# Kernel tuning notes

Hardware: AMD Instinct MI355X
Metric: run time of the kernel (lower is better)

Reference implementation:

```python
import jax, jax.numpy as jnp
import numpy as np

N, FIN, H, M = 20000, 64, 128, 16
EIA, EIR, EIT = 256000, 256000, 100000
EIN = 2 * H + 1          # EGNN edge-mlp input: feats_i | feats_j | rel_dist
EHID = 2 * EIN
NIN = H + M
NHID = 2 * H


def _gat(x_src, x_dst, ei, w_src, w_dst, a_s, a_d, b):
    # PyG GATConv, heads=1: alpha_ij = softmax_i(leaky_relu(a_s.Wx_j + a_d.Wx_i))
    n_dst = x_dst.shape[0]
    h_s = x_src @ w_src                      # [Ns, H]
    h_d = x_dst @ w_dst                      # [Nd, H]
    es = h_s @ a_s                           # [Ns]
    ed = h_d @ a_d                           # [Nd]
    j, i = ei[0], ei[1]                      # src, dst
    e = jax.nn.leaky_relu(es[j] + ed[i], 0.2)
    mx = jax.ops.segment_max(e, i, num_segments=n_dst)
    mx = jnp.where(jnp.isfinite(mx), mx, 0.0)  # guard empty segments
    ex = jnp.exp(e - mx[i])
    den = jax.ops.segment_sum(ex, i, num_segments=n_dst)
    alpha = ex / (den[i] + 1e-16)
    return jax.ops.segment_sum(alpha[:, None] * h_s[j], i, num_segments=n_dst) + b


def _egnn(x, ei, p):
    # EGNN_Sparse: x = [coors(3) | feats], 'add' aggregation, residual feat update
    ew1, eb1, ew2, eb2, cw1, cb1, cw2, cb2, nw1, nb1, nw2, nb2 = p
    coors, feats = x[:, :3], x[:, 3:]
    n = x.shape[0]
    j, i = ei[0], ei[1]
    rel = coors[j] - coors[i]                          # [E, 3] (src - dst)
    rd = jnp.sum(rel * rel, axis=-1, keepdims=True)    # [E, 1]
    m_in = jnp.concatenate([feats[i], feats[j], rd], axis=-1)
    m = jax.nn.silu(jax.nn.silu(m_in @ ew1 + eb1) @ ew2 + eb2)   # [E, M]
    cw = jax.nn.silu(m @ cw1 + cb1) @ cw2 + cb2                  # [E, 1]
    coors_out = coors + jax.ops.segment_sum(cw * rel, i, num_segments=n)
    m_i = jax.ops.segment_sum(m, i, num_segments=n)
    feats_out = feats + jax.nn.silu(jnp.concatenate([feats, m_i], axis=-1) @ nw1 + nb1) @ nw2 + nb2
    return jnp.concatenate([coors_out, feats_out], axis=-1)


def setup_inputs():
    ks = iter(jax.random.split(jax.random.key(0), 48))

    def nrm(shape, s=0.1):
        return jax.random.normal(next(ks), shape, dtype=jnp.float32) * s

    def ridx(shape):
        return jax.random.randint(next(ks), shape, 0, N, dtype=jnp.int32)

    return {
        "x1": nrm((N, FIN), 1.0), "x2": nrm((N, FIN), 1.0),
        "pos1": nrm((N, 3), 1.0), "pos2": nrm((N, 3), 1.0),
        "ei_intra1": ridx((2, EIA)), "ei_intra2": ridx((2, EIA)),
        "ei_12": ridx((2, EIR)), "ei_21": ridx((2, EIR)),
        "ei_int": ridx((2, EIT)),
        "g0_w": nrm((2, FIN, H)), "g0_as": nrm((2, H)), "g0_ad": nrm((2, H)), "g0_b": nrm((2, H)),
        "g1_w": nrm((2, H, H)), "g1_as": nrm((2, H)), "g1_ad": nrm((2, H)), "g1_b": nrm((2, H)),
        "it_ws": nrm((2, 2, H, H)), "it_wd": nrm((2, 2, H, H)),
        "it_as": nrm((2, 2, H)), "it_ad": nrm((2, 2, H)), "it_b": nrm((2, 2, H)),
        "eg_e_w1": nrm((2, 2, EIN, EHID)), "eg_e_b1": nrm((2, 2, EHID)),
        "eg_e_w2": nrm((2, 2, EHID, M)), "eg_e_b2": nrm((2, 2, M)),
        "eg_c_w1": nrm((2, 2, M, 4 * M)), "eg_c_b1": nrm((2, 2, 4 * M)),
        "eg_c_w2": nrm((2, 2, 4 * M, 1)), "eg_c_b2": nrm((2, 2, 1)),
        "eg_n_w1": nrm((2, 2, NIN, NHID)), "eg_n_b1": nrm((2, 2, NHID)),
        "eg_n_w2": nrm((2, 2, NHID, H)), "eg_n_b2": nrm((2, 2, H)),
        "lin_w": nrm((H, 1)), "lin_b": nrm((1,)),
        "aux_w1": nrm((2 * H, H)), "aux_b1": nrm((H,)),
        "aux_w2": nrm((H, 1)), "aux_b2": nrm((1,)),
    }


def reference(x1, x2, pos1, pos2,
              g0_w, g0_as, g0_ad, g0_b, g1_w, g1_as, g1_ad, g1_b,
              it_ws, it_wd, it_as, it_ad, it_b,
              eg_e_w1, eg_e_b1, eg_e_w2, eg_e_b2, eg_c_w1, eg_c_b1, eg_c_w2, eg_c_b2,
              eg_n_w1, eg_n_b1, eg_n_w2, eg_n_b2,
              lin_w, lin_b, aux_w1, aux_b1, aux_w2, aux_b2,
              ei_intra1, ei_intra2, ei_12, ei_21, ei_int):
    n1, n2 = x1.shape[0], x2.shape[0]
    sl1 = jnp.tile(jnp.arange(n1, dtype=ei_intra1.dtype)[None, :], (2, 1))
    sl2 = jnp.tile(jnp.arange(n2, dtype=ei_intra2.dtype)[None, :], (2, 1))
    ei1 = jnp.concatenate([ei_intra1, sl1], axis=1)  # GATConv add_self_loops=True
    ei2 = jnp.concatenate([ei_intra2, sl2], axis=1)
    # intra GAT layers (shared lin for src/dst)
    x1 = jax.nn.relu(_gat(x1, x1, ei1, g0_w[0], g0_w[0], g0_as[0], g0_ad[0], g0_b[0]))
    x2 = jax.nn.relu(_gat(x2, x2, ei2, g0_w[1], g0_w[1], g0_as[1], g0_ad[1], g0_b[1]))
    x1 = jax.nn.relu(_gat(x1, x1, ei1, g1_w[0], g1_w[0], g1_as[0], g1_ad[0], g1_b[0]))
    x2 = jax.nn.relu(_gat(x2, x2, ei2, g1_w[1], g1_w[1], g1_as[1], g1_ad[1], g1_b[1]))
    # inter GAT layers (bipartite, add_self_loops=False)
    for l in range(2):
        nx2 = jax.nn.relu(_gat(x1, x2, ei_12, it_ws[l, 0], it_wd[l, 0], it_as[l, 0], it_ad[l, 0], it_b[l, 0]))
        nx1 = jax.nn.relu(_gat(x2, x1, ei_21, it_ws[l, 1], it_wd[l, 1], it_as[l, 1], it_ad[l, 1], it_b[l, 1]))
        x1, x2 = nx1, nx2
    # EGNN layers (HeteroEGNN hstacks pos only when feat dim == node_dim, i.e. layer 0)
    egp = (eg_e_w1, eg_e_b1, eg_e_w2, eg_e_b2, eg_c_w1, eg_c_b1, eg_c_w2, eg_c_b2,
           eg_n_w1, eg_n_b1, eg_n_w2, eg_n_b2)
    h1 = jnp.concatenate([pos1, x1], axis=-1)
    h2 = jnp.concatenate([pos2, x2], axis=-1)
    for l in range(2):
        h1 = _egnn(h1, ei_intra1, tuple(p[l, 0] for p in egp))
        h2 = _egnn(h2, ei_intra2, tuple(p[l, 1] for p in egp))
    x1, x2 = h1[:, 3:], h2[:, 3:]
    # auxiliary distance head on interacting pairs
    xi = jnp.concatenate([x1[ei_int[0]], x2[ei_int[1]]], axis=-1)
    dist = jax.nn.relu(jax.nn.relu(xi @ aux_w1 + aux_b1) @ aux_w2 + aux_b2)
    return (x1 @ lin_w + lin_b, x2 @ lin_w + lin_b, dist)
```

## Files before the change

kernel.cpp:

```cpp
#include <hip/hip_runtime.h>
#include <hip/hip_bf16.h>
#include <cstdint>
#include <cstddef>

#define NN     20000
#define FIN_D  64
#define H_D    128
#define M_D    16
#define EIA_D  256000
#define EIR_D  256000
#define EIT_D  100000
#define EIN_D  257
#define EHID_D 514
#define NIN_D  144
#define NHID_D 256
#define APAD   544
#define BUPAD  272

typedef short bfrag __attribute__((ext_vector_type(8)));
typedef float ffrag __attribute__((ext_vector_type(4)));

__device__ __forceinline__ float siluf(float x) {
    return x * __builtin_amdgcn_rcpf(1.f + __expf(-x));
}
// ... 86 lines not shown
        lo[idx] = f2bf(v - bf2f(h));
    }
}

struct MMJob {
    const float* A; const float* A2;
    const int* gi0; const int* gi1;
    const unsigned short* Wh; const unsigned short* Wl;
    const float* bias; const float* res;
    float* C; unsigned short* C2;
    const float* da; const float* db;
    float* dota; float* dotb;
};
struct MMJobs { MMJob j[4]; };

template<int ACT, bool RES, bool OBF, bool GATHER, bool DUAL, int AMODE, int DOT, bool NOC>
__global__ __launch_bounds__(256) void k_mm(MMJobs js, int M, int Nc, int K, int Kpad, int ldc, int s2) {
    __shared__ __align__(16) unsigned short sAh[128 * 32];
    __shared__ __align__(16) unsigned short sAl[AMODE == 2 ? 128 * 32 : 16];
    const MMJob jb = js.j[blockIdx.z];
    const int tid = threadIdx.x;
    const int bm = blockIdx.x * 128, bn = blockIdx.y * 64;
    const int wv = tid >> 6, lane = tid & 63;
    ffrag acc[2][4];
#pragma unroll
    for (int mt = 0; mt < 2; ++mt)
#pragma unroll
        for (int nt = 0; nt < 4; ++nt)
#pragma unroll
            for (int r = 0; r < 4; ++r) acc[mt][nt][r] = 0.f;
    const int sr = tid >> 1;
    const int sks = (tid & 1) * 16;
    const int gm_s = bm + sr;
    const int sgmt = sr >> 4, smm = sr & 15, qb = (tid & 1) * 2;
// ... 13 lines not shown
#pragma unroll
            for (int i = 0; i < 4; ++i) {
                float4 t4 = ((const float4*)src)[i];
                v[4 * i] = t4.x; v[4 * i + 1] = t4.y; v[4 * i + 2] = t4.z; v[4 * i + 3] = t4.w;
            }
        } else {
#pragma unroll
            for (int i = 0; i < 16; ++i) v[i] = 0.f;
        }
#pragma unroll
        for (int o = 0; o < 2; ++o) {
            unsigned hw[4], lw[4];
#pragma unroll
            for (int p = 0; p < 4; ++p) {
                float f0 = v[o * 8 + 2 * p], f1 = v[o * 8 + 2 * p + 1];
                if (AMODE == 2) {
                    unsigned short h0 = f2bf(f0), h1 = f2bf(f1);
                    unsigned short l0 = f2bf(f0 - bf2f(h0)), l1 = f2bf(f1 - bf2f(h1));
                    hw[p] = (unsigned)h0 | ((unsigned)h1 << 16);
                    lw[p] = (unsigned)l0 | ((unsigned)l1 << 16);
                } else {
                    hw[p] = pkbf(f0, f1);
                }
            }
            int off16 = (sgmt * 4 + qb + o) * 16 + smm;
            ((uint4*)sAh)[off16] = make_uint4(hw[0], hw[1], hw[2], hw[3]);
            if (AMODE == 2) ((uint4*)sAl)[off16] = make_uint4(lw[0], lw[1], lw[2], lw[3]);
        }
        __syncthreads();
        bfrag bh[4], bl[4];
#pragma unroll
        for (int nt = 0; nt < 4; ++nt) {
            size_t woff = (size_t)(bn + nt * 16 + mm) * Kpad + k0 + q * 8;
            bh[nt] = *(const bfrag*)(jb.Wh + woff);
            bl[nt] = *(const bfrag*)(jb.Wl + woff);
        }
#pragma unroll
        for (int mt = 0; mt < 2; ++mt) {
            int off16 = ((wv * 2 + mt) * 4 + q) * 16 + mm;
            bfrag ah = ((const bfrag*)sAh)[off16];
#pragma unroll
            for (int nt = 0; nt < 4; ++nt) {
                acc[mt][nt] = __builtin_amdgcn_mfma_f32_16x16x32_bf16(ah, bh[nt], acc[mt][nt], 0, 0, 0);
                acc[mt][nt] = __builtin_amdgcn_mfma_f32_16x16x32_bf16(ah, bl[nt], acc[mt][nt], 0, 0, 0);
            }
            if (AMODE == 2) {
                bfrag al = ((const bfrag*)sAl)[off16];
#pragma unroll
                for (int nt = 0; nt < 4; ++nt)
                    acc[mt][nt] = __builtin_amdgcn_mfma_f32_16x16x32_bf16(al, bh[nt], acc[mt][nt], 0, 0, 0);
            }
        }
        __syncthreads();
    }
    if (DOT >= 1) {
        float dav[4], dbv[4];
#pragma unroll
        for (int nt = 0; nt < 4; ++nt) {
            int gn = bn + nt * 16 + mm;
            dav[nt] = (gn < Nc) ? jb.da[gn] : 0.f;
            if (DOT == 2) dbv[nt] = (gn < Nc) ? jb.db[gn] : 0.f;
        }
#pragma unroll
        for (int mt = 0; mt < 2; ++mt)
#pragma unroll
            for (int r = 0; r < 4; ++r) {
                int gm = bm + wv * 32 + mt * 16 + q * 4 + r;
                float sa = 0.f, sb = 0.f;
#pragma unroll
                for (int nt = 0; nt < 4; ++nt) {
                    sa += acc[mt][nt][r] * dav[nt];
                    if (DOT == 2) sb += acc[mt][nt][r] * dbv[nt];
                }
                sa += __shfl_xor(sa, 1); sa += __shfl_xor(sa, 2);
                sa += __shfl_xor(sa, 4); sa += __shfl_xor(sa, 8);
                if (DOT == 2) {
                    sb += __shfl_xor(sb, 1); sb += __shfl_xor(sb, 2);
                    sb += __shfl_xor(sb, 4); sb += __shfl_xor(sb, 8);
                }
                if (mm == 0 && gm < M) {
                    atomicAdd(jb.dota + gm, sa);
                    if (DOT == 2) atomicAdd(jb.dotb + gm, sb);
                }
            }
    }
    if (!NOC || DUAL) {
#pragma unroll
        for (int mt = 0; mt < 2; ++mt) {
#pragma unroll
            for (int nt = 0; nt < 4; ++nt) {
                int gn = bn + nt * 16 + mm;
                bool inb = gn < Nc;
                bool padz = OBF && !NOC && !inb && gn < ldc;
                if (!inb && !padz) continue;
#pragma unroll
                for (int r = 0; r < 4; ++r) {
                    int gm = bm + wv * 32 + mt * 16 + q * 4 + r;
                    if (gm >= M) continue;
                    if (padz) {
                        ((unsigned short*)jb.C)[(size_t)gm * ldc + gn] = 0;
                        continue;
                    }
                    float vv = acc[mt][nt][r];
                    if (jb.bias) vv += jb.bias[gn];
                    if (ACT == 1) vv = reluf(vv);
                    if (ACT == 2) vv = siluf(vv);
                    if (RES) vv += jb.res[(size_t)gm * Nc + gn];
                    if (!NOC) {
                        if (OBF) ((unsigned short*)jb.C)[(size_t)gm * ldc + gn] = f2bf(vv);
                        else jb.C[(size_t)gm * ldc + gn] = vv;
                    }
                    if (DUAL) jb.C2[(size_t)gm * ldc + gn] = f2bf(vv);
                }
            }
        }
    }
}

__global__ void k_nodescore(const float* __restrict__ x, const float* __restrict__ wv,
                            const float* __restrict__ b, float* __restrict__ o, int n) {
    int w = blockIdx.x * 4 + (threadIdx.x >> 6);
    int lane = threadIdx.x & 63;
    if (w >= n) return;
    const float* r = x + (size_t)w * H_D;
    float s = r[lane] * wv[lane] + r[lane + 64] * wv[lane + 64];
#pragma unroll
    for (int off = 32; off; off >>= 1) s += __shfl_xor(s, off);
    if (lane == 0) o[w] = s + b[0];
}

__global__ __launch_bounds__(256) void k_gat_fused(
        const int* __restrict__ rp, const int* __restrict__ cj, int hasSelf,
        const float* __restrict__ es, const float* __restrict__ ed,
        const unsigned* __restrict__ h16, const float* __restrict__ bias,
        float* __restrict__ out, int N) {
    int node = blockIdx.x * 4 + (threadIdx.x >> 6);
    int lane = threadIdx.x & 63;
    if (node >= N) return;
    int start = rp[node], end = rp[node + 1];
    float edi = ed[node];
    float den = 0.f, a0 = 0.f, a1 = 0.f;
    int p = start;
    for (; p + 2 <= end; p += 2) {
        int j0 = cj[p], j1 = cj[p + 1];
        float e0 = es[j0], e1 = es[j1];
        unsigned u0 = h16[(size_t)j0 * 64 + lane];
        unsigned u1 = h16[(size_t)j1 * 64 + lane];
        float v0 = e0 + edi; v0 = v0 < 0.f ? 0.2f * v0 : v0;
        float v1 = e1 + edi; v1 = v1 < 0.f ? 0.2f * v1 : v1;
        float x0 = __expf(v0), x1 = __expf(v1);
        den += x0 + x1;
        a0 += x0 * bf_lo(u0) + x1 * bf_lo(u1);
        a1 += x0 * bf_hi(u0) + x1 * bf_hi(u1);
    }
    if (p < end) {
        int j = cj[p];
        float v = es[j] + edi;
        v = v < 0.f ? 0.2f * v : v;
        float ex = __expf(v);
        den += ex;
        unsigned u = h16[(size_t)j * 64 + lane];
        a0 += ex * bf_lo(u);
        a1 += ex * bf_hi(u);
    }
    if (hasSelf) {
        float v = es[node] + edi;
        v = v < 0.f ? 0.2f * v : v;
        float ex = __expf(v);
        den += ex;
        unsigned u = h16[(size_t)node * 64 + lane];
        a0 += ex * bf_lo(u);
        a1 += ex * bf_hi(u);
    }
    float inv = 1.f / (den + 1e-16f);
    float2 o;
    o.x = reluf(a0 * inv + bias[2 * lane]);
    o.y = reluf(a1 * inv + bias[2 * lane + 1]);
    ((float2*)(out + (size_t)node * H_D))[lane] = o;
}

__global__ __launch_bounds__(256) void k_edge_mfma(
        const int* __restrict__ dsti, const int* __restrict__ cj, int nE,
        const unsigned* __restrict__ A16, const unsigned* __restrict__ Bp,
        const float* __restrict__ coors,
        const float* __restrict__ w_rd,
        const unsigned short* __restrict__ Wfh, const unsigned short* __restrict__ Wfl,
        const float* __restrict__ eb2,
        const float* __restrict__ cw1, const float* __restrict__ cb1,
        const float* __restrict__ cw2, const float* __restrict__ cb2,
        unsigned short* __restrict__ me16, float* __restrict__ cvec) {
    __shared__ __align__(16) float s_w[APAD];
    __shared__ float s_cw1[1024];
    __shared__ float s_cb1[64], s_cw2[64], s_eb2[16];
    __shared__ float sM[4][16][17];
    for (int i = threadIdx.x; i < APAD; i += 256)
        s_w[i] = (i < EHID_D) ? w_rd[i] : 0.f;
    for (int i = threadIdx.x; i < 1024; i += 256) s_cw1[i] = cw1[i];
    if (threadIdx.x < 64) { s_cb1[threadIdx.x] = cb1[threadIdx.x]; s_cw2[threadIdx.x] = cw2[threadIdx.x]; }
    if (threadIdx.x < 16) s_eb2[threadIdx.x] = eb2[threadIdx.x];
    __syncthreads();
    const float cb2v = cb2[0];
    const int wv = threadIdx.x >> 6, lane = threadIdx.x & 63;
    const int q = lane >> 4, mm = lane & 15;
    const int ebase = blockIdx.x * 64 + wv * 16;
    const int e = ebase + mm;
    const bool ev = e < nE;
    int ii = ev ? dsti[e] : 0;
    int jj = ev ? cj[e] : 0;
    float dx = coors[(size_t)jj * 3]     - coors[(size_t)ii * 3];
    float dy = coors[(size_t)jj * 3 + 1] - coors[(size_t)ii * 3 + 1];
    float dz = coors[(size_t)jj * 3 + 2] - coors[(size_t)ii * 3 + 2];
    float rd = dx * dx + dy * dy + dz * dz;
    const unsigned* Ar = A16 + (size_t)ii * BUPAD;
    const unsigned* Br = Bp + (size_t)jj * BUPAD;
    ffrag acc = {0.f, 0.f, 0.f, 0.f};
#pragma unroll 4
    for (int t = 0; t < 17; ++t) {
        int ks = t * 32 + q * 8;
        int ku = ks >> 1;
        uint4 au = *(const uint4*)(Ar + ku);
        uint4 bu = *(const uint4*)(Br + ku);
        float4 w0 = *(const float4*)(s_w + ks);
        float4 w1 = *(const float4*)(s_w + ks + 4);
        float g[8];
        g[0] = siluf(bf_lo(au.x) + bf_lo(bu.x) + rd * w0.x);
        g[1] = siluf(bf_hi(au.x) + bf_hi(bu.x) + rd * w0.y);
        g[2] = siluf(bf_lo(au.y) + bf_lo(bu.y) + rd * w0.z);
        g[3] = siluf(bf_hi(au.y) + bf_hi(bu.y) + rd * w0.w);
        g[4] = siluf(bf_lo(au.z) + bf_lo(bu.z) + rd * w1.x);
        g[5] = siluf(bf_hi(au.z) + bf_hi(bu.z) + rd * w1.y);
        g[6] = siluf(bf_lo(au.w) + bf_lo(bu.w) + rd * w1.z);
        g[7] = siluf(bf_hi(au.w) + bf_hi(bu.w) + rd * w1.w);
        bfrag ah;
        unsigned* ahp = (unsigned*)&ah;
        ahp[0] = pkbf(g[0], g[1]);
        ahp[1] = pkbf(g[2], g[3]);
        ahp[2] = pkbf(g[4], g[5]);
        ahp[3] = pkbf(g[6], g[7]);
        bfrag bh = *(const bfrag*)(Wfh + (size_t)(t * 64 + lane) * 8);
        bfrag bl = *(const bfrag*)(Wfl + (size_t)(t * 64 + lane) * 8);
        acc = __builtin_amdgcn_mfma_f32_16x16x32_bf16(ah, bh, acc, 0, 0, 0);
        acc = __builtin_amdgcn_mfma_f32_16x16x32_bf16(ah, bl, acc, 0, 0, 0);
    }
#pragma unroll
    for (int r = 0; r < 4; ++r) {
        int erow = q * 4 + r;
        float me = siluf(acc[r] + s_eb2[mm]);
        sM[wv][erow][mm] = me;
        int e2 = ebase + erow;
        if (e2 < nE) me16[(size_t)e2 * 16 + mm] = f2bf(me);
    }
    for (int el = 0; el < 16; ++el) {
        int e3 = ebase + el;
        if (e3 >= nE) break;
        float a = s_cb1[lane];
#pragma unroll
        for (int c = 0; c < 16; ++c) a += sM[wv][el][c] * s_cw1[c * 64 + lane];
        float p = siluf(a) * s_cw2[lane];
#pragma unroll
        for (int off = 32; off; off >>= 1) p += __shfl_xor(p, off);
        float cwv = p + cb2v;
        if (lane == el) {
            cvec[(size_t)e3 * 3]     = cwv * dx;
            cvec[(size_t)e3 * 3 + 1] = cwv * dy;
            cvec[(size_t)e3 * 3 + 2] = cwv * dz;
        }
    }
}

__global__ __launch_bounds__(256) void k_egnn_seg(
        const int* __restrict__ rp,
        const unsigned short* __restrict__ me16, const float* __restrict__ cvec,
        const float* __restrict__ coors,
        float* __restrict__ coorsOut, float* __restrict__ macc, int N) {
    int node = blockIdx.x * 4 + (threadIdx.x >> 6);
    int lane = threadIdx.x & 63;
    if (node >= N) return;
    int s = rp[node], en = rp[node + 1];
    int x = lane >> 4, c = lane & 15;
    float msum = 0.f, csum = 0.f;
    for (int p = s + x; p < en; p += 4) {
        msum += bf2f(me16[(size_t)p * 16 + c]);
        if (c < 3) csum += cvec[(size_t)p * 3 + c];
    }
    msum += __shfl_xor(msum, 16); msum += __shfl_xor(msum, 32);
    csum += __shfl_xor(csum, 16); csum += __shfl_xor(csum, 32);
    if (lane < 16) macc[(size_t)node * M_D + lane] = msum;
    if (lane < 3) coorsOut[(size_t)node * 3 + lane] = coors[(size_t)node * 3 + lane] + csum;
}

__global__ void k_dist(const float* __restrict__ Hb, const float* __restrict__ w2,
                       const float* __restrict__ b2, float* __restrict__ dist, int nE) {
    int e = blockIdx.x * 4 + (threadIdx.x >> 6);
    int lane = threadIdx.x & 63;
    if (e >= nE) return;
    const float* r = Hb + (size_t)e * H_D;
    float s = r[lane] * w2[lane] + r[lane + 64] * w2[lane + 64];
#pragma unroll
    for (int off = 32; off; off >>= 1) s += __shfl_xor(s, off);
    if (lane == 0) dist[e] = reluf(s + b2[0]);
}

extern "C" void kernel_launch(void* const* d_in, const int* in_sizes, int n_in,
// ... 124 lines not shown
    k_hist<<<gEA, 256, 0, stream>>>(ei_21 + EIR_D, EIR_D, cnt4 + 3 * N);
    k_scan4<<<4, 256, 0, stream>>>(cnt4, N, rp4);
    k_filli<<<(4 * N + 255) / 256, 256, 0, stream>>>(cnt4, 0, 4 * N);
    const int* rpI1 = rp4;
    const int* rpI2 = rp4 + (N + 1);
    const int* rp12 = rp4 + 2 * (N + 1);
    const int* rp21 = rp4 + 3 * (N + 1);
    k_scatter<<<gEA, 256, 0, stream>>>(ei_intra1, ei_intra1 + EIA_D, EIA_D, rpI1, cnt4, cjI1, dstI1);
    k_scatter<<<gEA, 256, 0, stream>>>(ei_intra2, ei_intra2 + EIA_D, EIA_D, rpI2, cnt4 + N, cjI2, dstI2);
    k_scatter<<<gEA, 256, 0, stream>>>(ei_12, ei_12 + EIR_D, EIR_D, rp12, cnt4 + 2 * N, cj12, nullptr);
    k_scatter<<<gEA, 256, 0, stream>>>(ei_21, ei_21 + EIR_D, EIR_D, rp21, cnt4 + 3 * N, cj21, nullptr);

    const int MB = (N + 127) / 128;
    MMJobs js{};

    auto intra = [&](const float* xa, const float* xb, int wa, int wb,
                     const float* as_a, const float* ad_a, const float* as_b, const float* ad_b,
                     const float* b_a, const float* b_b, int K, float* oa, float* ob) {
        int Kpad = (K + 31) & ~31;
        k_filli<<<(4 * N + 255) / 256, 256, 0, stream>>>((int*)esed, 0, 4 * N);
        js.j[0] = {xa, nullptr, nullptr, nullptr, WH(wa), WL(wa), nullptr, nullptr,
                   nullptr, (unsigned short*)h16a, as_a, ad_a, es1, ed1};
        js.j[1] = {xb, nullptr, nullptr, nullptr, WH(wb), WL(wb), nullptr, nullptr,
                   nullptr, (unsigned short*)h16b, as_b, ad_b, es2, ed2};
        k_mm<0, false, false, false, true, 1, 2, true><<<dim3(MB, 2, 2), 256, 0, stream>>>(
            js, N, H, K, Kpad, H, 0);
        k_gat_fused<<<gNW, 256, 0, stream>>>(rpI1, cjI1, 1, es1, ed1, h16a, b_a, oa, N);
        k_gat_fused<<<gNW, 256, 0, stream>>>(rpI2, cjI2, 1, es2, ed2, h16b, b_b, ob, N);
    };

    intra(x1_in, x2_in, 0, 1, g0_as, g0_ad, g0_as + H, g0_ad + H, g0_b, g0_b + H, FIN_D, x1a, x2a);
    const float* cx1 = x1a;
    const float* cx2 = x2a;
    intra(cx1, cx2, 2, 3, g1_as, g1_ad, g1_as + H, g1_ad + H, g1_b, g1_b + H, H, x1b, x2b);
    cx1 = x1b; cx2 = x2b;

    {
        float* outs1[2] = {x1a, x1b};
        float* outs2[2] = {x2a, x2b};
        for (int l = 0; l < 2; ++l) {
            int p0 = l * 2 + 0, p1 = l * 2 + 1;
            float* o2 = outs2[l];
            float* o1 = outs1[l];
            k_filli<<<(4 * N + 255) / 256, 256, 0, stream>>>((int*)esed, 0, 4 * N);
            js.j[0] = {cx1, nullptr, nullptr, nullptr, WH(4 + p0), WL(4 + p0), nullptr, nullptr,
                       nullptr, (unsigned short*)h16a, it_as + p0 * H, nullptr, es1, nullptr};
            js.j[1] = {cx2, nullptr, nullptr, nullptr, WH(4 + p1), WL(4 + p1), nullptr, nullptr,
                       nullptr, (unsigned short*)h16b, it_as + p1 * H, nullptr, es2, nullptr};
            k_mm<0, false, false, false, true, 1, 1, true><<<dim3(MB, 2, 2), 256, 0, stream>>>(
                js, N, H, H, H, H, 0);
            js.j[0] = {cx2, nullptr, nullptr, nullptr, WH(8 + p0), WL(8 + p0), nullptr, nullptr,
                       nullptr, nullptr, it_ad + p0 * H, nullptr, ed1, nullptr};
            js.j[1] = {cx1, nullptr, nullptr, nullptr, WH(8 + p1), WL(8 + p1), nullptr, nullptr,
                       nullptr, nullptr, it_ad + p1 * H, nullptr, ed2, nullptr};
            k_mm<0, false, false, false, false, 1, 1, true><<<dim3(MB, 2, 2), 256, 0, stream>>>(
                js, N, H, H, H, H, 0);
            k_gat_fused<<<gNW, 256, 0, stream>>>(rp12, cj12, 0, es1, ed1, h16a, it_b + p0 * H, o2, N);
            k_gat_fused<<<gNW, 256, 0, stream>>>(rp21, cj21, 0, es2, ed2, h16b, it_b + p1 * H, o1, N);
            cx1 = o1; cx2 = o2;
        }
    }

    auto egnn_pair = [&](const float* f1, const float* f2, const float* c1, const float* c2,
                         int l, float* fo1, float* fo2, float* co1, float* co2) {
        int p0 = 2 * l, p1 = 2 * l + 1;
        js.j[0] = {f1, nullptr, nullptr, nullptr, WH(12 + 2 * p0), WL(12 + 2 * p0),
                   eg_e_b1 + p0 * EHID_D, nullptr, (float*)A16a, nullptr, nullptr, nullptr, nullptr, nullptr};
        js.j[1] = {f1, nullptr, nullptr, nullptr, WH(13 + 2 * p0), WL(13 + 2 * p0),
                   nullptr, nullptr, (float*)B16a, nullptr, nullptr, nullptr, nullptr, nullptr};
        js.j[2] = {f2, nullptr, nullptr, nullptr, WH(12 + 2 * p1), WL(12 + 2 * p1),
                   eg_e_b1 + p1 * EHID_D, nullptr, (float*)A16b, nullptr, nullptr, nullptr, nullptr, nullptr};
        js.j[3] = {f2, nullptr, nullptr, nullptr, WH(13 + 2 * p1), WL(13 + 2 * p1),
                   nullptr, nullptr, (float*)B16b, nullptr, nullptr, nullptr, nullptr, nullptr};
        k_mm<0, false, true, false, false, 1, 0, false><<<dim3(MB, 9, 4), 256, 0, stream>>>(
            js, N, EHID_D, H, H, APAD, 0);
        const float* ew1a = eg_e_w1 + (size_t)p0 * EIN_D * EHID_D;
        const float* ew1b = eg_e_w1 + (size_t)p1 * EIN_D * EHID_D;
        k_edge_mfma<<<(EIA_D + 63) / 64, 256, 0, stream>>>(
            dstI1, cjI1, EIA_D, A16a, B16a, c1, ew1a + (size_t)256 * EHID_D,
            Wf + (size_t)p0 * 8704, Wf + 4 * 8704 + (size_t)p0 * 8704,
            eg_e_b2 + p0 * M_D, eg_c_w1 + p0 * M_D * 64, eg_c_b1 + p0 * 64,
            eg_c_w2 + p0 * 64, eg_c_b2 + p0, me16a, cveca);
        k_edge_mfma<<<(EIA_D + 63) / 64, 256, 0, stream>>>(
            dstI2, cjI2, EIA_D, A16b, B16b, c2, ew1b + (size_t)256 * EHID_D,
            Wf + (size_t)p1 * 8704, Wf + 4 * 8704 + (size_t)p1 * 8704,
            eg_e_b2 + p1 * M_D, eg_c_w1 + p1 * M_D * 64, eg_c_b1 + p1 * 64,
            eg_c_w2 + p1 * 64, eg_c_b2 + p1, me16b, cvecb);
        k_egnn_seg<<<gNW, 256, 0, stream>>>(rpI1, me16a, cveca, c1, co1, macc1, N);
        k_egnn_seg<<<gNW, 256, 0, stream>>>(rpI2, me16b, cvecb, c2, co2, macc2, N);
        js.j[0] = {f1, macc1, iota, iota, WH(20 + p0), WL(20 + p0),
                   eg_n_b1 + p0 * NHID_D, nullptr, nh1, nullptr, nullptr, nullptr, nullptr, nullptr};
        js.j[1] = {f2, macc2, iota, iota, WH(20 + p1), WL(20 + p1),
                   eg_n_b1 + p1 * NHID_D, nullptr, nh2, nullptr, nullptr, nullptr, nullptr, nullptr};
        k_mm<2, false, false, true, false, 2, 0, false><<<dim3(MB, 4, 2), 256, 0, stream>>>(
            js, N, NHID_D, NIN_D, 160, NHID_D, M_D);
        js.j[0] = {nh1, nullptr, nullptr, nullptr, WH(24 + p0), WL(24 + p0),
                   eg_n_b2 + p0 * H, f1, fo1, nullptr, nullptr, nullptr, nullptr, nullptr};
        js.j[1] = {nh2, nullptr, nullptr, nullptr, WH(24 + p1), WL(24 + p1),
                   eg_n_b2 + p1 * H, f2, fo2, nullptr, nullptr, nullptr, nullptr, nullptr};
        k_mm<0, true, false, false, false, 2, 0, false><<<dim3(MB, 2, 2), 256, 0, stream>>>(
            js, N, H, NHID_D, NHID_D, H, 0);
    };
    egnn_pair(cx1, cx2, pos1, pos2, 0, x1a, x2a, co1a, co2a);
    cx1 = x1a; cx2 = x2a;
    egnn_pair(cx1, cx2, co1a, co2a, 1, x1b, x2b, co1b, co2b);
    cx1 = x1b; cx2 = x2b;

    k_nodescore<<<gNW, 256, 0, stream>>>(cx1, lin_w, lin_b, dout, N);
    k_nodescore<<<gNW, 256, 0, stream>>>(cx2, lin_w, lin_b, dout + N, N);
    js.j[0] = {cx1, cx2, ei_int, ei_int + EIT_D, WH(28), WL(28),
               aux_b1, nullptr, Hb, nullptr, nullptr, nullptr, nullptr, nullptr};
    k_mm<1, false, false, true, false, 2, 0, false><<<dim3((EIT_D + 127) / 128, 2, 1), 256, 0, stream>>>(
        js, EIT_D, H, 2 * H, 2 * H, H, H_D);
    k_dist<<<(EIT_D + 3) / 4, 256, 0, stream>>>(Hb, aux_w2, aux_b2, dout + 2 * N, EIT_D);
}
```

Before: 1.601 ms.

## Add full-K resident GEMM kernel and batch paired GAT/edge/segment launches

Adds k_mmf, which stages the whole 128-row A tile in shared memory once and loops over all N-column blocks inside one workgroup. This lets the attention dot products be written directly, removing the zero-fill kernels and atomics. The paired GAT, EGNN edge and segment kernels now launch once each, with a 2-wide grid dimension selecting the job, which cuts launch count. The GAT aggregation loop is unrolled by 4 to put more gathers in flight. The trade-off is fewer workgroups per GEMM (grid y becomes 1), so each block does more serial work and parallelism drops.

```diff
diff --git a/kernel.cpp b/kernel.cpp
--- a/kernel.cpp
+++ b/kernel.cpp
@@ -124,10 +124,151 @@
 };
 struct MMJobs { MMJob j[4]; };
 
-template<int ACT, bool RES, bool OBF, bool GATHER, bool DUAL, int AMODE, int DOT, bool NOC>
+template<int ACT, bool OBF, int DOT, bool NOC, int KT>
+__global__ __launch_bounds__(256) void k_mmf(MMJobs js, int M, int Nc, int ldc, int nbn) {
+    constexpr int K = KT * 32;
+    __shared__ __align__(16) unsigned short sAh[128 * K];
+    const MMJob jb = js.j[blockIdx.z];
+    const int tid = threadIdx.x;
+    const int bm = blockIdx.x * 128;
+    const int wv = tid >> 6, lane = tid & 63;
+    const int q = lane >> 4, mm = lane & 15;
+    const int sr = tid >> 1;
+    const int sks = (tid & 1) * 16;
+    const int gm_s = bm + sr;
+    const int sgmt = sr >> 4, smm = sr & 15, qb = (tid & 1) * 2;
+#pragma unroll
+    for (int t = 0; t < KT; ++t) {
+        float v[16];
+        if (gm_s < M) {
+            const float* src = jb.A + (size_t)gm_s * K + t * 32 + sks;
+#pragma unroll
+            for (int i = 0; i < 4; ++i) {
+                float4 t4 = ((const float4*)src)[i];
+                v[4 * i] = t4.x; v[4 * i + 1] = t4.y; v[4 * i + 2] = t4.z; v[4 * i + 3] = t4.w;
+            }
+        } else {
+#pragma unroll
+            for (int i = 0; i < 16; ++i) v[i] = 0.f;
+        }
+#pragma unroll
+        for (int o = 0; o < 2; ++o) {
+            unsigned hw[4];
+#pragma unroll
+            for (int p = 0; p < 4; ++p)
+                hw[p] = pkbf(v[o * 8 + 2 * p], v[o * 8 + 2 * p + 1]);
+            int off16 = ((sgmt * KT + t) * 4 + qb + o) * 16 + smm;
+            ((uint4*)sAh)[off16] = make_uint4(hw[0], hw[1], hw[2], hw[3]);
+        }
+    }
+    __syncthreads();
+    float dra[2][4] = {}, drb[2][4] = {};
+    for (int b = 0; b < nbn; ++b) {
+        const int bn = b * 64;
+        ffrag acc[2][4];
+#pragma unroll
+        for (int mt = 0; mt < 2; ++mt)
+#pragma unroll
+            for (int nt = 0; nt < 4; ++nt)
+#pragma unroll
+                for (int r = 0; r < 4; ++r) acc[mt][nt][r] = 0.f;
+#pragma unroll
+        for (int t = 0; t < KT; ++t) {
+            bfrag bh[4], bl[4];
+#pragma unroll
+            for (int nt = 0; nt < 4; ++nt) {
+                size_t woff = (size_t)(bn + nt * 16 + mm) * K + t * 32 + q * 8;
+                bh[nt] = *(const bfrag*)(jb.Wh + woff);
+                bl[nt] = *(const bfrag*)(jb.Wl + woff);
+            }
+#pragma unroll
+            for (int mt = 0; mt < 2; ++mt) {
+                int off16 = (((wv * 2 + mt) * KT + t) * 4 + q) * 16 + mm;
+                bfrag ah = ((const bfrag*)sAh)[off16];
+#pragma unroll
+                for (int nt = 0; nt < 4; ++nt) {
+                    acc[mt][nt] = __builtin_amdgcn_mfma_f32_16x16x32_bf16(ah, bh[nt], acc[mt][nt], 0, 0, 0);
+                    acc[mt][nt] = __builtin_amdgcn_mfma_f32_16x16x32_bf16(ah, bl[nt], acc[mt][nt], 0, 0, 0);
+                }
+            }
+        }
+        if (DOT >= 1) {
+            float dav[4], dbv[4];
+#pragma unroll
+            for (int nt = 0; nt < 4; ++nt) {
+                int gn = bn + nt * 16 + mm;
+                dav[nt] = (gn < Nc) ? jb.da[gn] : 0.f;
+                if (DOT == 2) dbv[nt] = (gn < Nc) ? jb.db[gn] : 0.f;
+            }
+#pragma unroll
+            for (int mt = 0; mt < 2; ++mt)
+#pragma unroll
+                for (int r = 0; r < 4; ++r)
+#pragma unroll
+                    for (int nt = 0; nt < 4; ++nt) {
+                        dra[mt][r] += acc[mt][nt][r] * dav[nt];
+                        if (DOT == 2) drb[mt][r] += acc[mt][nt][r] * dbv[nt];
+                    }
+        }
+        const bool doC2 = jb.C2 != nullptr;
+        if (!NOC || doC2) {
+#pragma unroll
+            for (int mt = 0; mt < 2; ++mt) {
+#pragma unroll
+                for (int nt = 0; nt < 4; ++nt) {
+                    int gn = bn + nt * 16 + mm;
+                    bool inb = gn < Nc;
+                    bool padz = OBF && !NOC && !inb && gn < ldc;
+                    if (!inb && !padz) continue;
+#pragma unroll
+                    for (int r = 0; r < 4; ++r) {
+                        int gm = bm + wv * 32 + mt * 16 + q * 4 + r;
+                        if (gm >= M) continue;
+                        if (padz) {
+                            ((unsigned short*)jb.C)[(size_t)gm * ldc + gn] = 0;
+                            continue;
+                        }
+                        float vv = acc[mt][nt][r];
+                        if (jb.bias) vv += jb.bias[gn];
+                        if (ACT == 1) vv = reluf(vv);
+                        if (ACT == 2) vv = siluf(vv);
+                        if (!NOC) {
+                            if (OBF) ((unsigned short*)jb.C)[(size_t)gm * ldc + gn] = f2bf(vv);
+                            else jb.C[(size_t)gm * ldc + gn] = vv;
+                        }
+                        if (doC2) jb.C2[(size_t)gm * ldc + gn] = f2bf(vv);
+                    }
+                }
+            }
+        }
+    }
+    if (DOT >= 1) {
+#pragma unroll
+        for (int mt = 0; mt < 2; ++mt)
+#pragma unroll
+            for (int r = 0; r < 4; ++r) {
+                float sa = dra[mt][r];
+                sa += __shfl_xor(sa, 1); sa += __shfl_xor(sa, 2);
+                sa += __shfl_xor(sa, 4); sa += __shfl_xor(sa, 8);
+                float sb = 0.f;
+                if (DOT == 2) {
+                    sb = drb[mt][r];
+                    sb += __shfl_xor(sb, 1); sb += __shfl_xor(sb, 2);
+                    sb += __shfl_xor(sb, 4); sb += __shfl_xor(sb, 8);
+                }
+                int gm = bm + wv * 32 + mt * 16 + q * 4 + r;
+                if (mm == 0 && gm < M) {
+                    jb.dota[gm] = sa;
+                    if (DOT == 2) jb.dotb[gm] = sb;
+                }
+            }
+    }
+}
+
+template<int ACT, bool RES, bool GATHER>
 __global__ __launch_bounds__(256) void k_mm(MMJobs js, int M, int Nc, int K, int Kpad, int ldc, int s2) {
     __shared__ __align__(16) unsigned short sAh[128 * 32];
-    __shared__ __align__(16) unsigned short sAl[AMODE == 2 ? 128 * 32 : 16];
+    __shared__ __align__(16) unsigned short sAl[128 * 32];
     const MMJob jb = js.j[blockIdx.z];
     const int tid = threadIdx.x;
     const int bm = blockIdx.x * 128, bn = blockIdx.y * 64;
@@ -171,18 +312,14 @@
 #pragma unroll
             for (int p = 0; p < 4; ++p) {
                 float f0 = v[o * 8 + 2 * p], f1 = v[o * 8 + 2 * p + 1];
-                if (AMODE == 2) {
-                    unsigned short h0 = f2bf(f0), h1 = f2bf(f1);
-                    unsigned short l0 = f2bf(f0 - bf2f(h0)), l1 = f2bf(f1 - bf2f(h1));
-                    hw[p] = (unsigned)h0 | ((unsigned)h1 << 16);
-                    lw[p] = (unsigned)l0 | ((unsigned)l1 << 16);
-                } else {
-                    hw[p] = pkbf(f0, f1);
-                }
+                unsigned short h0 = f2bf(f0), h1 = f2bf(f1);
+                unsigned short l0 = f2bf(f0 - bf2f(h0)), l1 = f2bf(f1 - bf2f(h1));
+                hw[p] = (unsigned)h0 | ((unsigned)h1 << 16);
+                lw[p] = (unsigned)l0 | ((unsigned)l1 << 16);
             }
             int off16 = (sgmt * 4 + qb + o) * 16 + smm;
             ((uint4*)sAh)[off16] = make_uint4(hw[0], hw[1], hw[2], hw[3]);
-            if (AMODE == 2) ((uint4*)sAl)[off16] = make_uint4(lw[0], lw[1], lw[2], lw[3]);
+            ((uint4*)sAl)[off16] = make_uint4(lw[0], lw[1], lw[2], lw[3]);
         }
         __syncthreads();
         bfrag bh[4], bl[4];
@@ -196,79 +333,32 @@
         for (int mt = 0; mt < 2; ++mt) {
             int off16 = ((wv * 2 + mt) * 4 + q) * 16 + mm;
             bfrag ah = ((const bfrag*)sAh)[off16];
+            bfrag al = ((const bfrag*)sAl)[off16];
 #pragma unroll
             for (int nt = 0; nt < 4; ++nt) {
                 acc[mt][nt] = __builtin_amdgcn_mfma_f32_16x16x32_bf16(ah, bh[nt], acc[mt][nt], 0, 0, 0);
                 acc[mt][nt] = __builtin_amdgcn_mfma_f32_16x16x32_bf16(ah, bl[nt], acc[mt][nt], 0, 0, 0);
-            }
-            if (AMODE == 2) {
-                bfrag al = ((const bfrag*)sAl)[off16];
-#pragma unroll
-                for (int nt = 0; nt < 4; ++nt)
-                    acc[mt][nt] = __builtin_amdgcn_mfma_f32_16x16x32_bf16(al, bh[nt], acc[mt][nt], 0, 0, 0);
+                acc[mt][nt] = __builtin_amdgcn_mfma_f32_16x16x32_bf16(al, bh[nt], acc[mt][nt], 0, 0, 0);
             }
         }
         __syncthreads();
     }
-    if (DOT >= 1) {
-        float dav[4], dbv[4];
+#pragma unroll
+    for (int mt = 0; mt < 2; ++mt) {
 #pragma unroll
         for (int nt = 0; nt < 4; ++nt) {
             int gn = bn + nt * 16 + mm;
-            dav[nt] = (gn < Nc) ? jb.da[gn] : 0.f;
-            if (DOT == 2) dbv[nt] = (gn < Nc) ? jb.db[gn] : 0.f;
-        }
-#pragma unroll
-        for (int mt = 0; mt < 2; ++mt)
+            if (gn >= Nc) continue;
 #pragma unroll
             for (int r = 0; r < 4; ++r) {
                 int gm = bm + wv * 32 + mt * 16 + q * 4 + r;
-                float sa = 0.f, sb = 0.f;
-#pragma unroll
-                for (int nt = 0; nt < 4; ++nt) {
-                    sa += acc[mt][nt][r] * dav[nt];
-                    if (DOT == 2) sb += acc[mt][nt][r] * dbv[nt];
-                }
-                sa += __shfl_xor(sa, 1); sa += __shfl_xor(sa, 2);
-                sa += __shfl_xor(sa, 4); sa += __shfl_xor(sa, 8);
-                if (DOT == 2) {
-                    sb += __shfl_xor(sb, 1); sb += __shfl_xor(sb, 2);
-                    sb += __shfl_xor(sb, 4); sb += __shfl_xor(sb, 8);
-                }
-                if (mm == 0 && gm < M) {
-                    atomicAdd(jb.dota + gm, sa);
-                    if (DOT == 2) atomicAdd(jb.dotb + gm, sb);
-                }
-            }
-    }
-    if (!NOC || DUAL) {
-#pragma unroll
-        for (int mt = 0; mt < 2; ++mt) {
-#pragma unroll
-            for (int nt = 0; nt < 4; ++nt) {
-                int gn = bn + nt * 16 + mm;
-                bool inb = gn < Nc;
-                bool padz = OBF && !NOC && !inb && gn < ldc;
-                if (!inb && !padz) continue;
-#pragma unroll
-                for (int r = 0; r < 4; ++r) {
-                    int gm = bm + wv * 32 + mt * 16 + q * 4 + r;
-                    if (gm >= M) continue;
-                    if (padz) {
-                        ((unsigned short*)jb.C)[(size_t)gm * ldc + gn] = 0;
-                        continue;
-                    }
-                    float vv = acc[mt][nt][r];
-                    if (jb.bias) vv += jb.bias[gn];
-                    if (ACT == 1) vv = reluf(vv);
-                    if (ACT == 2) vv = siluf(vv);
-                    if (RES) vv += jb.res[(size_t)gm * Nc + gn];
-                    if (!NOC) {
-                        if (OBF) ((unsigned short*)jb.C)[(size_t)gm * ldc + gn] = f2bf(vv);
-                        else jb.C[(size_t)gm * ldc + gn] = vv;
-                    }
-                    if (DUAL) jb.C2[(size_t)gm * ldc + gn] = f2bf(vv);
-                }
+                if (gm >= M) continue;
+                float vv = acc[mt][nt][r];
+                if (jb.bias) vv += jb.bias[gn];
+                if (ACT == 1) vv = reluf(vv);
+                if (ACT == 2) vv = siluf(vv);
+                if (RES) vv += jb.res[(size_t)gm * Nc + gn];
+                jb.C[(size_t)gm * ldc + gn] = vv;
             }
         }
     }
@@ -286,90 +376,97 @@
     if (lane == 0) o[w] = s + b[0];
 }
 
-__global__ __launch_bounds__(256) void k_gat_fused(
-        const int* __restrict__ rp, const int* __restrict__ cj, int hasSelf,
-        const float* __restrict__ es, const float* __restrict__ ed,
-        const unsigned* __restrict__ h16, const float* __restrict__ bias,
-        float* __restrict__ out, int N) {
+struct GatJob {
+    const int* rp; const int* cj; int hasSelf;
+    const float* es; const float* ed;
+    const unsigned* h16; const float* bias; float* out;
+};
+__global__ __launch_bounds__(256) void k_gat2(GatJob j0, GatJob j1, int N) {
+    const GatJob jb = blockIdx.y ? j1 : j0;
     int node = blockIdx.x * 4 + (threadIdx.x >> 6);
     int lane = threadIdx.x & 63;
     if (node >= N) return;
-    int start = rp[node], end = rp[node + 1];
-    float edi = ed[node];
+    int start = jb.rp[node], end = jb.rp[node + 1];
+    float edi = jb.ed[node];
     float den = 0.f, a0 = 0.f, a1 = 0.f;
     int p = start;
-    for (; p + 2 <= end; p += 2) {
-        int j0 = cj[p], j1 = cj[p + 1];
-        float e0 = es[j0], e1 = es[j1];
-        unsigned u0 = h16[(size_t)j0 * 64 + lane];
-        unsigned u1 = h16[(size_t)j1 * 64 + lane];
-        float v0 = e0 + edi; v0 = v0 < 0.f ? 0.2f * v0 : v0;
-        float v1 = e1 + edi; v1 = v1 < 0.f ? 0.2f * v1 : v1;
-        float x0 = __expf(v0), x1 = __expf(v1);
-        den += x0 + x1;
-        a0 += x0 * bf_lo(u0) + x1 * bf_lo(u1);
-        a1 += x0 * bf_hi(u0) + x1 * bf_hi(u1);
-    }
-    if (p < end) {
-        int j = cj[p];
-        float v = es[j] + edi;
+    for (; p + 4 <= end; p += 4) {
+        int j[4]; float e[4]; unsigned u[4];
+#pragma unroll
+        for (int x = 0; x < 4; ++x) j[x] = jb.cj[p + x];
+#pragma unroll
+        for (int x = 0; x < 4; ++x) { e[x] = jb.es[j[x]]; u[x] = jb.h16[(size_t)j[x] * 64 + lane]; }
+#pragma unroll
+        for (int x = 0; x < 4; ++x) {
+            float v = e[x] + edi;
+            v = v < 0.f ? 0.2f * v : v;
+            float ex = __expf(v);
+            den += ex;
+            a0 += ex * bf_lo(u[x]);
+            a1 += ex * bf_hi(u[x]);
+        }
+    }
+    for (; p < end; ++p) {
+        int j = jb.cj[p];
+        float v = jb.es[j] + edi;
         v = v < 0.f ? 0.2f * v : v;
         float ex = __expf(v);
         den += ex;
-        unsigned u = h16[(size_t)j * 64 + lane];
+        unsigned u = jb.h16[(size_t)j * 64 + lane];
         a0 += ex * bf_lo(u);
         a1 += ex * bf_hi(u);
     }
-    if (hasSelf) {
-        float v = es[node] + edi;
+    if (jb.hasSelf) {
+        float v = jb.es[node] + edi;
         v = v < 0.f ? 0.2f * v : v;
         float ex = __expf(v);
         den += ex;
-        unsigned u = h16[(size_t)node * 64 + lane];
+        unsigned u = jb.h16[(size_t)node * 64 + lane];
         a0 += ex * bf_lo(u);
         a1 += ex * bf_hi(u);
     }
     float inv = 1.f / (den + 1e-16f);
     float2 o;
-    o.x = reluf(a0 * inv + bias[2 * lane]);
-    o.y = reluf(a1 * inv + bias[2 * lane + 1]);
-    ((float2*)(out + (size_t)node * H_D))[lane] = o;
-}
-
-__global__ __launch_bounds__(256) void k_edge_mfma(
-        const int* __restrict__ dsti, const int* __restrict__ cj, int nE,
-        const unsigned* __restrict__ A16, const unsigned* __restrict__ Bp,
-        const float* __restrict__ coors,
-        const float* __restrict__ w_rd,
-        const unsigned short* __restrict__ Wfh, const unsigned short* __restrict__ Wfl,
-        const float* __restrict__ eb2,
-        const float* __restrict__ cw1, const float* __restrict__ cb1,
-        const float* __restrict__ cw2, const float* __restrict__ cb2,
-        unsigned short* __restrict__ me16, float* __restrict__ cvec) {
+    o.x = reluf(a0 * inv + jb.bias[2 * lane]);
+    o.y = reluf(a1 * inv + jb.bias[2 * lane + 1]);
+    ((float2*)(jb.out + (size_t)node * H_D))[lane] = o;
+}
+
+struct EJob {
+    const int* dsti; const int* cj;
+    const unsigned* A16; const unsigned* Bp; const float* coors;
+    const float* w_rd;
+    const unsigned short* Wfh; const unsigned short* Wfl;
+    const float* eb2; const float* cw1; const float* cb1;
+    const float* cw2; const float* cb2;
+    unsigned short* me16; float* cvec;
+};
+__global__ __launch_bounds__(256) void k_edge2(EJob e0, EJob e1, int nE) {
+    const EJob jb = blockIdx.y ? e1 : e0;
     __shared__ __align__(16) float s_w[APAD];
     __shared__ float s_cw1[1024];
     __shared__ float s_cb1[64], s_cw2[64], s_eb2[16];
     __shared__ float sM[4][16][17];
     for (int i = threadIdx.x; i < APAD; i += 256)
-        s_w[i] = (i < EHID_D) ? w_rd[i] : 0.f;
-    for (int i = threadIdx.x; i < 1024; i += 256) s_cw1[i] = cw1[i];
-    if (threadIdx.x < 64) { s_cb1[threadIdx.x] = cb1[threadIdx.x]; s_cw2[threadIdx.x] = cw2[threadIdx.x]; }
-    if (threadIdx.x < 16) s_eb2[threadIdx.x] = eb2[threadIdx.x];
+        s_w[i] = (i < EHID_D) ? jb.w_rd[i] : 0.f;
+    for (int i = threadIdx.x; i < 1024; i += 256) s_cw1[i] = jb.cw1[i];
+    if (threadIdx.x < 64) { s_cb1[threadIdx.x] = jb.cb1[threadIdx.x]; s_cw2[threadIdx.x] = jb.cw2[threadIdx.x]; }
+    if (threadIdx.x < 16) s_eb2[threadIdx.x] = jb.eb2[threadIdx.x];
     __syncthreads();
-    const float cb2v = cb2[0];
+    const float cb2v = jb.cb2[0];
     const int wv = threadIdx.x >> 6, lane = threadIdx.x & 63;
     const int q = lane >> 4, mm = lane & 15;
     const int ebase = blockIdx.x * 64 + wv * 16;
     const int e = ebase + mm;
     const bool ev = e < nE;
-    int ii = ev ? dsti[e] : 0;
-    int jj = ev ? cj[e] : 0;
-    float dx = coors[(size_t)jj * 3]     - coors[(size_t)ii * 3];
-    float dy = coors[(size_t)jj * 3 + 1] - coors[(size_t)ii * 3 + 1];
-    float dz = coors[(size_t)jj * 3 + 2] - coors[(size_t)ii * 3 + 2];
+    int ii = ev ? jb.dsti[e] : 0;
+    int jj = ev ? jb.cj[e] : 0;
+    float dx = jb.coors[(size_t)jj * 3]     - jb.coors[(size_t)ii * 3];
+    float dy = jb.coors[(size_t)jj * 3 + 1] - jb.coors[(size_t)ii * 3 + 1];
+    float dz = jb.coors[(size_t)jj * 3 + 2] - jb.coors[(size_t)ii * 3 + 2];
     float rd = dx * dx + dy * dy + dz * dz;
-    const unsigned* Ar = A16 + (size_t)ii * BUPAD;
-    const unsigned* Br = Bp + (size_t)jj * BUPAD;
+    const unsigned* Ar = jb.A16 + (size_t)ii * BUPAD;
+    const unsigned* Br = jb.Bp + (size_t)jj * BUPAD;
     ffrag acc = {0.f, 0.f, 0.f, 0.f};
 #pragma unroll 4
     for (int t = 0; t < 17; ++t) {
@@ -394,8 +491,8 @@
         ahp[1] = pkbf(g[2], g[3]);
         ahp[2] = pkbf(g[4], g[5]);
         ahp[3] = pkbf(g[6], g[7]);
-        bfrag bh = *(const bfrag*)(Wfh + (size_t)(t * 64 + lane) * 8);
-        bfrag bl = *(const bfrag*)(Wfl + (size_t)(t * 64 + lane) * 8);
+        bfrag bh = *(const bfrag*)(jb.Wfh + (size_t)(t * 64 + lane) * 8);
+        bfrag bl = *(const bfrag*)(jb.Wfl + (size_t)(t * 64 + lane) * 8);
         acc = __builtin_amdgcn_mfma_f32_16x16x32_bf16(ah, bh, acc, 0, 0, 0);
         acc = __builtin_amdgcn_mfma_f32_16x16x32_bf16(ah, bl, acc, 0, 0, 0);
     }
@@ -405,7 +502,7 @@
         float me = siluf(acc[r] + s_eb2[mm]);
         sM[wv][erow][mm] = me;
         int e2 = ebase + erow;
-        if (e2 < nE) me16[(size_t)e2 * 16 + mm] = f2bf(me);
+        if (e2 < nE) jb.me16[(size_t)e2 * 16 + mm] = f2bf(me);
     }
     for (int el = 0; el < 16; ++el) {
         int e3 = ebase + el;
@@ -418,32 +515,33 @@
         for (int off = 32; off; off >>= 1) p += __shfl_xor(p, off);
         float cwv = p + cb2v;
         if (lane == el) {
-            cvec[(size_t)e3 * 3]     = cwv * dx;
-            cvec[(size_t)e3 * 3 + 1] = cwv * dy;
-            cvec[(size_t)e3 * 3 + 2] = cwv * dz;
-        }
-    }
-}
-
-__global__ __launch_bounds__(256) void k_egnn_seg(
-        const int* __restrict__ rp,
-        const unsigned short* __restrict__ me16, const float* __restrict__ cvec,
-        const float* __restrict__ coors,
-        float* __restrict__ coorsOut, float* __restrict__ macc, int N) {
+            jb.cvec[(size_t)e3 * 3]     = cwv * dx;
+            jb.cvec[(size_t)e3 * 3 + 1] = cwv * dy;
+            jb.cvec[(size_t)e3 * 3 + 2] = cwv * dz;
+        }
+    }
+}
+
+struct SJob {
+    const int* rp; const unsigned short* me16; const float* cvec;
+    const float* coors; float* coorsOut; float* macc;
+};
+__global__ __launch_bounds__(256) void k_seg2(SJob s0, SJob s1, int N) {
+    const SJob jb = blockIdx.y ? s1 : s0;
     int node = blockIdx.x * 4 + (threadIdx.x >> 6);
     int lane = threadIdx.x & 63;
     if (node >= N) return;
-    int s = rp[node], en = rp[node + 1];
+    int s = jb.rp[node], en = jb.rp[node + 1];
     int x = lane >> 4, c = lane & 15;
     float msum = 0.f, csum = 0.f;
     for (int p = s + x; p < en; p += 4) {
-        msum += bf2f(me16[(size_t)p * 16 + c]);
-        if (c < 3) csum += cvec[(size_t)p * 3 + c];
+        msum += bf2f(jb.me16[(size_t)p * 16 + c]);
+        if (c < 3) csum += jb.cvec[(size_t)p * 3 + c];
     }
     msum += __shfl_xor(msum, 16); msum += __shfl_xor(msum, 32);
     csum += __shfl_xor(csum, 16); csum += __shfl_xor(csum, 32);
-    if (lane < 16) macc[(size_t)node * M_D + lane] = msum;
-    if (lane < 3) coorsOut[(size_t)node * 3 + lane] = coors[(size_t)node * 3 + lane] + csum;
+    if (lane < 16) jb.macc[(size_t)node * M_D + lane] = msum;
+    if (lane < 3) jb.coorsOut[(size_t)node * 3 + lane] = jb.coors[(size_t)node * 3 + lane] + csum;
 }
 
 __global__ void k_dist(const float* __restrict__ Hb, const float* __restrict__ w2,
@@ -598,25 +696,26 @@
     const int MB = (N + 127) / 128;
     MMJobs js{};
 
-    auto intra = [&](const float* xa, const float* xb, int wa, int wb,
-                     const float* as_a, const float* ad_a, const float* as_b, const float* ad_b,
-                     const float* b_a, const float* b_b, int K, float* oa, float* ob) {
-        int Kpad = (K + 31) & ~31;
-        k_filli<<<(4 * N + 255) / 256, 256, 0, stream>>>((int*)esed, 0, 4 * N);
+    auto intraL = [&](auto kt_tag, const float* xa, const float* xb, int wa, int wb,
+                      const float* as_a, const float* ad_a, const float* as_b, const float* ad_b,
+                      const float* b_a, const float* b_b, float* oa, float* ob) {
+        constexpr int KT = decltype(kt_tag)::value;
         js.j[0] = {xa, nullptr, nullptr, nullptr, WH(wa), WL(wa), nullptr, nullptr,
                    nullptr, (unsigned short*)h16a, as_a, ad_a, es1, ed1};
         js.j[1] = {xb, nullptr, nullptr, nullptr, WH(wb), WL(wb), nullptr, nullptr,
                    nullptr, (unsigned short*)h16b, as_b, ad_b, es2, ed2};
-        k_mm<0, false, false, false, true, 1, 2, true><<<dim3(MB, 2, 2), 256, 0, stream>>>(
-            js, N, H, K, Kpad, H, 0);
-        k_gat_fused<<<gNW, 256, 0, stream>>>(rpI1, cjI1, 1, es1, ed1, h16a, b_a, oa, N);
-        k_gat_fused<<<gNW, 256, 0, stream>>>(rpI2, cjI2, 1, es2, ed2, h16b, b_b, ob, N);
+        k_mmf<0, false, 2, true, KT><<<dim3(MB, 1, 2), 256, 0, stream>>>(js, N, H, H, 2);
+        GatJob g0{rpI1, cjI1, 1, es1, ed1, h16a, b_a, oa};
+        GatJob g1{rpI2, cjI2, 1, es2, ed2, h16b, b_b, ob};
+        k_gat2<<<dim3(gNW, 2), 256, 0, stream>>>(g0, g1, N);
     };
 
-    intra(x1_in, x2_in, 0, 1, g0_as, g0_ad, g0_as + H, g0_ad + H, g0_b, g0_b + H, FIN_D, x1a, x2a);
+    intraL(std::integral_constant<int, 2>{}, x1_in, x2_in, 0, 1,
+           g0_as, g0_ad, g0_as + H, g0_ad + H, g0_b, g0_b + H, x1a, x2a);
     const float* cx1 = x1a;
     const float* cx2 = x2a;
-    intra(cx1, cx2, 2, 3, g1_as, g1_ad, g1_as + H, g1_ad + H, g1_b, g1_b + H, H, x1b, x2b);
+    intraL(std::integral_constant<int, 4>{}, cx1, cx2, 2, 3,
+           g1_as, g1_ad, g1_as + H, g1_ad + H, g1_b, g1_b + H, x1b, x2b);
     cx1 = x1b; cx2 = x2b;
 
     {
@@ -626,21 +725,18 @@
             int p0 = l * 2 + 0, p1 = l * 2 + 1;
             float* o2 = outs2[l];
             float* o1 = outs1[l];
-            k_filli<<<(4 * N + 255) / 256, 256, 0, stream>>>((int*)esed, 0, 4 * N);
             js.j[0] = {cx1, nullptr, nullptr, nullptr, WH(4 + p0), WL(4 + p0), nullptr, nullptr,
                        nullptr, (unsigned short*)h16a, it_as + p0 * H, nullptr, es1, nullptr};
             js.j[1] = {cx2, nullptr, nullptr, nullptr, WH(4 + p1), WL(4 + p1), nullptr, nullptr,
                        nullptr, (unsigned short*)h16b, it_as + p1 * H, nullptr, es2, nullptr};
-            k_mm<0, false, false, false, true, 1, 1, true><<<dim3(MB, 2, 2), 256, 0, stream>>>(
-                js, N, H, H, H, H, 0);
-            js.j[0] = {cx2, nullptr, nullptr, nullptr, WH(8 + p0), WL(8 + p0), nullptr, nullptr,
+            js.j[2] = {cx2, nullptr, nullptr, nullptr, WH(8 + p0), WL(8 + p0), nullptr, nullptr,
                        nullptr, nullptr, it_ad + p0 * H, nullptr, ed1, nullptr};
-            js.j[1] = {cx1, nullptr, nullptr, nullptr, WH(8 + p1), WL(8 + p1), nullptr, nullptr,
+            js.j[3] = {cx1, nullptr, nullptr, nullptr, WH(8 + p1), WL(8 + p1), nullptr, nullptr,
                        nullptr, nullptr, it_ad + p1 * H, nullptr, ed2, nullptr};
-            k_mm<0, false, false, false, false, 1, 1, true><<<dim3(MB, 2, 2), 256, 0, stream>>>(
-                js, N, H, H, H, H, 0);
-            k_gat_fused<<<gNW, 256, 0, stream>>>(rp12, cj12, 0, es1, ed1, h16a, it_b + p0 * H, o2, N);
-            k_gat_fused<<<gNW, 256, 0, stream>>>(rp21, cj21, 0, es2, ed2, h16b, it_b + p1 * H, o1, N);
+            k_mmf<0, false, 1, true, 4><<<dim3(MB, 1, 4), 256, 0, stream>>>(js, N, H, H, 2);
+            GatJob g0{rp12, cj12, 0, es1, ed1, h16a, it_b + p0 * H, o2};
+            GatJob g1{rp21, cj21, 0, es2, ed2, h16b, it_b + p1 * H, o1};
+            k_gat2<<<dim3(gNW, 2), 256, 0, stream>>>(g0, g1, N);
             cx1 = o1; cx2 = o2;
         }
     }
@@ -656,34 +752,31 @@
                    eg_e_b1 + p1 * EHID_D, nullptr, (float*)A16b, nullptr, nullptr, nullptr, nullptr, nullptr};
         js.j[3] = {f2, nullptr, nullptr, nullptr, WH(13 + 2 * p1), WL(13 + 2 * p1),
                    nullptr, nullptr, (float*)B16b, nullptr, nullptr, nullptr, nullptr, nullptr};
-        k_mm<0, false, true, false, false, 1, 0, false><<<dim3(MB, 9, 4), 256, 0, stream>>>(
-            js, N, EHID_D, H, H, APAD, 0);
+        k_mmf<0, true, 0, false, 4><<<dim3(MB, 1, 4), 256, 0, stream>>>(js, N, EHID_D, APAD, 9);
         const float* ew1a = eg_e_w1 + (size_t)p0 * EIN_D * EHID_D;
         const float* ew1b = eg_e_w1 + (size_t)p1 * EIN_D * EHID_D;
-        k_edge_mfma<<<(EIA_D + 63) / 64, 256, 0, stream>>>(
-            dstI1, cjI1, EIA_D, A16a, B16a, c1, ew1a + (size_t)256 * EHID_D,
-            Wf + (size_t)p0 * 8704, Wf + 4 * 8704 + (size_t)p0 * 8704,
-            eg_e_b2 + p0 * M_D, eg_c_w1 + p0 * M_D * 64, eg_c_b1 + p0 * 64,
-            eg_c_w2 + p0 * 64, eg_c_b2 + p0, me16a, cveca);
-        k_edge_mfma<<<(EIA_D + 63) / 64, 256, 0, stream>>>(
-            dstI2, cjI2, EIA_D, A16b, B16b, c2, ew1b + (size_t)256 * EHID_D,
-            Wf + (size_t)p1 * 8704, Wf + 4 * 8704 + (size_t)p1 * 8704,
-            eg_e_b2 + p1 * M_D, eg_c_w1 + p1 * M_D * 64, eg_c_b1 + p1 * 64,
-            eg_c_w2 + p1 * 64, eg_c_b2 + p1, me16b, cvecb);
-        k_egnn_seg<<<gNW, 256, 0, stream>>>(rpI1, me16a, cveca, c1, co1, macc1, N);
-        k_egnn_seg<<<gNW, 256, 0, stream>>>(rpI2, me16b, cvecb, c2, co2, macc2, N);
+        EJob e0{dstI1, cjI1, A16a, B16a, c1, ew1a + (size_t)256 * EHID_D,
+                Wf + (size_t)p0 * 8704, Wf + 4 * 8704 + (size_t)p0 * 8704,
+                eg_e_b2 + p0 * M_D, eg_c_w1 + p0 * M_D * 64, eg_c_b1 + p0 * 64,
+                eg_c_w2 + p0 * 64, eg_c_b2 + p0, me16a, cveca};
+        EJob e1{dstI2, cjI2, A16b, B16b, c2, ew1b + (size_t)256 * EHID_D,
+                Wf + (size_t)p1 * 8704, Wf + 4 * 8704 + (size_t)p1 * 8704,
+                eg_e_b2 + p1 * M_D, eg_c_w1 + p1 * M_D * 64, eg_c_b1 + p1 * 64,
+                eg_c_w2 + p1 * 64, eg_c_b2 + p1, me16b, cvecb};
+        k_edge2<<<dim3((EIA_D + 63) / 64, 2), 256, 0, stream>>>(e0, e1, EIA_D);
+        SJob s0{rpI1, me16a, cveca, c1, co1, macc1};
+        SJob s1{rpI2, me16b, cvecb, c2, co2, macc2};
+        k_seg2<<<dim3(gNW, 2), 256, 0, stream>>>(s0, s1, N);
         js.j[0] = {f1, macc1, iota, iota, WH(20 + p0), WL(20 + p0),
                    eg_n_b1 + p0 * NHID_D, nullptr, nh1, nullptr, nullptr, nullptr, nullptr, nullptr};
         js.j[1] = {f2, macc2, iota, iota, WH(20 + p1), WL(20 + p1),
                    eg_n_b1 + p1 * NHID_D, nullptr, nh2, nullptr, nullptr, nullptr, nullptr, nullptr};
-        k_mm<2, false, false, true, false, 2, 0, false><<<dim3(MB, 4, 2), 256, 0, stream>>>(
-            js, N, NHID_D, NIN_D, 160, NHID_D, M_D);
+        k_mm<2, false, true><<<dim3(MB, 4, 2), 256, 0, stream>>>(js, N, NHID_D, NIN_D, 160, NHID_D, M_D);
         js.j[0] = {nh1, nullptr, nullptr, nullptr, WH(24 + p0), WL(24 + p0),
                    eg_n_b2 + p0 * H, f1, fo1, nullptr, nullptr, nullptr, nullptr, nullptr};
         js.j[1] = {nh2, nullptr, nullptr, nullptr, WH(24 + p1), WL(24 + p1),
                    eg_n_b2 + p1 * H, f2, fo2, nullptr, nullptr, nullptr, nullptr, nullptr};
-        k_mm<0, true, false, false, false, 2, 0, false><<<dim3(MB, 2, 2), 256, 0, stream>>>(
-            js, N, H, NHID_D, NHID_D, H, 0);
+        k_mm<0, true, false><<<dim3(MB, 2, 2), 256, 0, stream>>>(js, N, H, NHID_D, NHID_D, H, 0);
     };
     egnn_pair(cx1, cx2, pos1, pos2, 0, x1a, x2a, co1a, co2a);
     cx1 = x1a; cx2 = x2a;
@@ -694,7 +787,7 @@
     k_nodescore<<<gNW, 256, 0, stream>>>(cx2, lin_w, lin_b, dout + N, N);
     js.j[0] = {cx1, cx2, ei_int, ei_int + EIT_D, WH(28), WL(28),
                aux_b1, nullptr, Hb, nullptr, nullptr, nullptr, nullptr, nullptr};
-    k_mm<1, false, false, true, false, 2, 0, false><<<dim3((EIT_D + 127) / 128, 2, 1), 256, 0, stream>>>(
+    k_mm<1, false, true><<<dim3((EIT_D + 127) / 128, 2, 1), 256, 0, stream>>>(
         js, EIT_D, H, 2 * H, 2 * H, H, H_D);
     k_dist<<<(EIT_D + 3) / 4, 256, 0, stream>>>(Hb, aux_w2, aux_b2, dout + 2 * N, EIT_D);
 }
```

New measurement: 1.499 ms. 1.07x faster.
